# Performance work log

Hardware: AMD Instinct MI355X
Metric: run time of the kernel (lower is better)

## Reference

```python
import jax, jax.numpy as jnp
import numpy as np

N_NODES = 100000


def gcn_conv(x, W, b, src, dst, dinv):
    # PyG GCNConv with default add_self_loops=True, symmetric normalization.
    # x: [N, Fin], W: [Fin, Fout]. Self-loop contribution handled analytically
    # (norm for loop edge i->i is dinv[i]^2) instead of materializing loop edges.
    xw = x @ W                                   # [N, Fout]
    norm = dinv[src] * dinv[dst]                 # [E]
    msgs = xw[src] * norm[:, None]               # [E, Fout]
    agg = jax.ops.segment_sum(msgs, dst, num_segments=N_NODES)
    agg = agg + xw * (dinv * dinv)[:, None]      # self-loops
    return agg + b


def setup_inputs() -> dict:
    key = jax.random.key(0)
    ks = jax.random.split(key, 12)
    E = 3200000
    S = 1000000
    F_in = 512
    x = jax.random.normal(ks[0], (N_NODES, F_in), dtype=jnp.float32)
    edge_index = jax.random.randint(ks[1], (2, E), 0, N_NODES, dtype=jnp.int64)
    samples = jax.random.randint(ks[2], (S, 2), 0, N_NODES, dtype=jnp.int64)

    def glorot(k, fi, fo):
        lim = float(np.sqrt(6.0 / (fi + fo)))
        return jax.random.uniform(k, (fi, fo), jnp.float32, -lim, lim)

    W1 = glorot(ks[3], F_in, 8)
    b1 = jnp.zeros((8,), jnp.float32)
    W2 = glorot(ks[4], 8, 16)
    b2 = jnp.zeros((16,), jnp.float32)
    W3 = glorot(ks[5], 16, 32)
    b3 = jnp.zeros((32,), jnp.float32)
    Wfc = glorot(ks[6], 64, 1)
    bfc = jnp.zeros((1,), jnp.float32)
    return {"x": x, "edge_index": edge_index, "samples": samples,
            "W1": W1, "b1": b1, "W2": W2, "b2": b2, "W3": W3, "b3": b3,
            "Wfc": Wfc, "bfc": bfc}


def reference(x, edge_index, samples, W1, b1, W2, b2, W3, b3, Wfc, bfc):
    src, dst = edge_index[0], edge_index[1]
    # degree with self-loops (edge weight 1), deg >= 1 so rsqrt is safe
    deg = jax.ops.segment_sum(jnp.ones_like(src, dtype=x.dtype), dst,
                              num_segments=N_NODES) + 1.0
    dinv = jax.lax.rsqrt(deg)
    h = jax.nn.relu(gcn_conv(x, W1, b1, src, dst, dinv))
    h = jax.nn.relu(gcn_conv(h, W2, b2, src, dst, dinv))
    h = gcn_conv(h, W3, b3, src, dst, dinv)
    x_i = h[samples[:, 0]]                       # [S, 32]
    x_j = h[samples[:, 1]]                       # [S, 32]
    x_ij = jnp.concatenate([x_i, x_j], axis=1)   # [S, 64]
    return jax.nn.sigmoid(x_ij @ Wfc + bfc).squeeze(-1)
```

## Files before the change

kernel.cpp:

```cpp
#include <hip/hip_runtime.h>
#include <cstdint>

#define N_NODES 100000
#define NBKT 2048
#define KNODE 49
#define NBLK 256
#define TPB_P 512
#define CAP  2048


__global__ void k_hist(const int* __restrict__ dst, int* __restrict__ hist, int E) {
    __shared__ int h[NBKT];
    for (int i = threadIdx.x; i < NBKT; i += blockDim.x) h[i] = 0;
    __syncthreads();
    int chunk = (E + NBLK - 1) / NBLK;
    int lo = blockIdx.x * chunk, hi = min(lo + chunk, E);
    for (int i = lo + threadIdx.x; i < hi; i += blockDim.x)
        atomicAdd(&h[dst[i] / KNODE], 1);
    __syncthreads();
    int* hr = hist + (size_t)blockIdx.x * NBKT;
    for (int i = threadIdx.x; i < NBKT; i += blockDim.x) hr[i] = h[i];
}


__global__ void k_offs(const int* __restrict__ hist, int* __restrict__ offs,
                       int* __restrict__ btot) {
    int bkt = (blockIdx.x * blockDim.x + threadIdx.x) >> 6;
    if (bkt >= NBKT) return;
    int lane = threadIdx.x & 63;
    int vals[4], loc[4];
    int s = 0;
#pragma unroll
    for (int j = 0; j < 4; ++j) {
        int rr = lane * 4 + j;
        int r = ((rr & 31) << 3) | (rr >> 5);
        vals[j] = hist[(size_t)r * NBKT + bkt];
        loc[j] = s;
        s += vals[j];
    }
    int inc = s;
#pragma unroll
    for (int off = 1; off < 64; off <<= 1) {
        int u = __shfl_up(inc, off);
        if (lane >= off) inc += u;
    }
    int excl = inc - s;
#pragma unroll
    for (int j = 0; j < 4; ++j) {
        int rr = lane * 4 + j;
        int r = ((rr & 31) << 3) | (rr >> 5);
        offs[(size_t)r * NBKT + bkt] = excl + loc[j];
    }
    if (lane == 63) btot[bkt] = excl + s;
}


__global__ void k_bktscan(const int* __restrict__ btot, int* __restrict__ bbase) {
    __shared__ int s[256];
    int t = threadIdx.x;
    int loc[8];
    int sum = 0;
#pragma unroll
    for (int j = 0; j < 8; ++j) { loc[j] = btot[t * 8 + j]; sum += loc[j]; }
    s[t] = sum;
    __syncthreads();
    for (int off = 1; off < 256; off <<= 1) {
        int v = (t >= off) ? s[t - off] : 0;
        __syncthreads();
        s[t] += v;
        __syncthreads();
    }
    int base = s[t] - sum;
#pragma unroll
    for (int j = 0; j < 8; ++j) { bbase[t * 8 + j] = base; base += loc[j]; }
    if (t == 255) bbase[NBKT] = base;
}


__global__ void k_place(const int* __restrict__ src, const int* __restrict__ dst,
                        const int* __restrict__ offs, const int* __restrict__ bbase,
                        int* __restrict__ tmp, int E) {
    __shared__ int cur[NBKT];
    const int* orow = offs + (size_t)blockIdx.x * NBKT;
    for (int i = threadIdx.x; i < NBKT; i += blockDim.x) cur[i] = bbase[i] + orow[i];
    __syncthreads();
    int chunk = (E + NBLK - 1) / NBLK;
    int lo = blockIdx.x * chunk, hi = min(lo + chunk, E);
    for (int i = lo + threadIdx.x; i < hi; i += blockDim.x) {
        int d = dst[i], s = src[i];
        int b = d / KNODE;
        int p = atomicAdd(&cur[b], 1);
        tmp[p] = (s << 6) | (d - b * KNODE);
    }
}


__global__ void k_finalize(const int* __restrict__ tmp, const int* __restrict__ bbase,
                           int* __restrict__ row_start, float* __restrict__ dinv,
                           int* __restrict__ csr, int n) {
    __shared__ int sE[CAP];
    __shared__ int cnt[KNODE];
    __shared__ int pfx[KNODE];
    __shared__ int cur[KNODE];
    int b = blockIdx.x;
    int t = threadIdx.x;
    for (int i = t; i < KNODE; i += blockDim.x) cnt[i] = 0;
    __syncthreads();
    int n0 = bbase[b], n1 = bbase[b + 1];
    int m = n1 - n0;
    for (int i = t; i < m; i += blockDim.x) {
        int e = tmp[n0 + i];
        if (i < CAP) sE[i] = e;
        atomicAdd(&cnt[e & 63], 1);
    }
    __syncthreads();
    if (t == 0) {
        int run = n0;
        for (int j = 0; j < KNODE; ++j) { pfx[j] = run; run += cnt[j]; }
    }
    __syncthreads();
    if (t < KNODE) {
        int node = b * KNODE + t;
        if (node < n) {
            row_start[node] = pfx[t];
            dinv[node] = rsqrtf((float)cnt[t] + 1.0f);
        }
        cur[t] = pfx[t];
    }
    if (b == 0 && t == 0) row_start[n] = bbase[NBKT];
    __syncthreads();
    for (int i = t; i < m; i += blockDim.x) {
        int e = (i < CAP) ? sE[i] : tmp[n0 + i];
        int pos = atomicAdd(&cur[e & 63], 1);
        csr[pos] = e >> 6;
    }
}


__global__ void k_gemm1(const float* __restrict__ x, const float* __restrict__ W,
                        const float* __restrict__ dinv, float* __restrict__ xw, int n) {
    __shared__ float sWT[8 * 512];
    for (int i = threadIdx.x; i < 4096; i += blockDim.x) {
        int k = i >> 3, c = i & 7;
        sWT[c * 512 + k] = W[i];
    }
    __syncthreads();
    int wid = (blockIdx.x * blockDim.x + threadIdx.x) >> 6;
    int lane = threadIdx.x & 63;
    int r_sub = lane >> 3, j = lane & 7;
    int row = wid * 8 + r_sub;
    if (row >= n) return;
    const float* xr = x + (size_t)row * 512;
    float acc[8];
#pragma unroll
    for (int c = 0; c < 8; ++c) acc[c] = 0.f;
#pragma unroll 4
    for (int it = 0; it < 16; ++it) {
        int kb = it * 32 + j * 4;
        float4 v = *(const float4*)(xr + kb);
#pragma unroll
        for (int c = 0; c < 8; ++c) {
            const float* wt = &sWT[c * 512 + kb];
            acc[c] += v.x * wt[0] + v.y * wt[1] + v.z * wt[2] + v.w * wt[3];
        }
    }
#pragma unroll
    for (int off = 1; off < 8; off <<= 1)
#pragma unroll
        for (int c = 0; c < 8; ++c)
            acc[c] += __shfl_xor(acc[c], off);
    float outv = acc[0];
#pragma unroll
    for (int c = 1; c < 8; ++c) if (j == c) outv = acc[c];
    xw[(size_t)row * 8 + j] = outv * dinv[row];
}


__global__ void k_gather1(const float* __restrict__ xw, const int* __restrict__ csr,
                          const int* __restrict__ row_start, const float* __restrict__ dinv,
                          const float* __restrict__ b, float* __restrict__ out, int n) {
    int wid = (blockIdx.x * blockDim.x + threadIdx.x) >> 6;
    int lane = threadIdx.x & 63;
    if (wid >= n) return;
    int e = lane >> 3, c = lane & 7;
    int k0 = row_start[wid], k1 = row_start[wid + 1];
    float acc = 0.f;
    for (int k = k0 + e; k < k1; k += 8)
        acc += xw[(size_t)csr[k] * 8 + c];
    if (e == 0) acc += xw[(size_t)wid * 8 + c];
#pragma unroll
    for (int off = 8; off < 64; off <<= 1) acc += __shfl_xor(acc, off);
    if (lane < 8) {
        float di = dinv[wid];
        out[(size_t)wid * 8 + c] = fmaxf(acc * di + b[c], 0.f) * di;
    }
}


__global__ void k_gather2(const float* __restrict__ h1, const int* __restrict__ csr,
                          const int* __restrict__ row_start, const float* __restrict__ dinv,
                          const float* __restrict__ W2, const float* __restrict__ b2,
                          float* __restrict__ h2, int n) {
    __shared__ float sW[8 * 16];
    __shared__ float sB[16];
    if (threadIdx.x < 128) sW[threadIdx.x] = W2[threadIdx.x];
    if (threadIdx.x < 16) sB[threadIdx.x] = b2[threadIdx.x];
    __syncthreads();
    int wid = (blockIdx.x * blockDim.x + threadIdx.x) >> 6;
    int lane = threadIdx.x & 63;
    if (wid >= n) return;
    int e = lane >> 3, c = lane & 7;
    int k0 = row_start[wid], k1 = row_start[wid + 1];
    float acc = 0.f;
    for (int k = k0 + e; k < k1; k += 8)
        acc += h1[(size_t)csr[k] * 8 + c];
    if (e == 0) acc += h1[(size_t)wid * 8 + c];
#pragma unroll
    for (int off = 8; off < 64; off <<= 1) acc += __shfl_xor(acc, off);
    float di = dinv[wid];
    acc *= di;
    float s2[8];
#pragma unroll
    for (int k = 0; k < 8; ++k) s2[k] = __shfl(acc, k);
    if (lane < 16) {
        float a = sB[lane];
#pragma unroll
        for (int k = 0; k < 8; ++k) a += s2[k] * sW[k * 16 + lane];
        h2[(size_t)wid * 16 + lane] = fmaxf(a, 0.f) * di;
    }
}


__global__ void k_gather3(const float* __restrict__ h2, const int* __restrict__ csr,
                          const int* __restrict__ row_start, const float* __restrict__ dinv,
                          const float* __restrict__ v, const float* __restrict__ ch,
                          float* __restrict__ pi, float* __restrict__ pj, int n) {
    int wid = (blockIdx.x * blockDim.x + threadIdx.x) >> 6;
    int lane = threadIdx.x & 63;
    if (wid >= n) return;
    int e = lane >> 4, c = lane & 15;
    int k0 = row_start[wid], k1 = row_start[wid + 1];
    float acc = 0.f;
    for (int k = k0 + e; k < k1; k += 4)
        acc += h2[(size_t)csr[k] * 16 + c];
    if (e == 0) acc += h2[(size_t)wid * 16 + c];
#pragma unroll
    for (int off = 16; off < 64; off <<= 1) acc += __shfl_xor(acc, off);
    float t = acc * v[c];
    float u = acc * v[16 + c];
#pragma unroll
    for (int off = 1; off < 16; off <<= 1) {
        t += __shfl_xor(t, off);
        u += __shfl_xor(u, off);
    }
    if (lane == 0) {
        float di = dinv[wid];
        pi[wid] = t * di + ch[0];
        pj[wid] = u * di + ch[1];
    }
}


__global__ void k_prep_head(const float* __restrict__ W3, const float* __restrict__ b3,
                            const float* __restrict__ Wfc, float* __restrict__ v,
                            float* __restrict__ c) {
    int t = threadIdx.x;
    if (t < 32) {
        int j = t & 15;
        const float* wf = Wfc + (t < 16 ? 0 : 32);
        float a = 0.f;
        for (int k = 0; k < 32; ++k) a += W3[j * 32 + k] * wf[k];
        v[t] = a;
    } else if (t < 34) {
        const float* wf = Wfc + (t == 32 ? 0 : 32);
        float a = 0.f;
        for (int k = 0; k < 32; ++k) a += b3[k] * wf[k];
        c[t - 32] = a;
    }
}


__global__ void k_samples_fast(const int2* __restrict__ samples, const float* __restrict__ pi,
                               const float* __restrict__ pj, const float* __restrict__ bfc,
                               float* __restrict__ out, int S) {
    int i = blockIdx.x * blockDim.x + threadIdx.x;
    if (i >= S) return;
    int2 s = samples[i];
    float z = pi[s.x] + pj[s.y] + bfc[0];
    out[i] = 1.0f / (1.0f + __expf(-z));
}


extern "C" void kernel_launch(void* const* d_in, const int* in_sizes, int n_in,
                              void* d_out, int out_size, void* d_ws, size_t ws_size,
                              hipStream_t stream) {
    const float* x   = (const float*)d_in[0];
    const int*   ei  = (const int*)d_in[1];
    const int*   smp = (const int*)d_in[2];
    const float* W1  = (const float*)d_in[3];
    const float* b1  = (const float*)d_in[4];
    const float* W2  = (const float*)d_in[5];
    const float* b2  = (const float*)d_in[6];
    const float* W3  = (const float*)d_in[7];
    const float* b3  = (const float*)d_in[8];
    const float* Wfc = (const float*)d_in[9];
    const float* bfc = (const float*)d_in[10];
    float* out = (float*)d_out;

    const int E = in_sizes[1] / 2;
    const int S = in_sizes[2] / 2;
    const int N = N_NODES;
    const int* src = ei;
    const int* dst = ei + E;

    char* w = (char*)d_ws;
    size_t off = 0;
    auto alloc = [&](size_t bytes) {
        char* p = w + off;
        off += (bytes + 255) & ~(size_t)255;
        return p;
    };
    int*   row_start = (int*)alloc((N + 1) * 4);
    float* dinv      = (float*)alloc(N * 4);
    int*   csr       = (int*)alloc((size_t)E * 4);
    int*   btot      = (int*)alloc(NBKT * 4);
    int*   bbase     = (int*)alloc((NBKT + 1) * 4);

    size_t off_layers = off;
    float* xw1       = (float*)alloc((size_t)N * 8 * 4);
    float* h1        = (float*)alloc((size_t)N * 8 * 4);
    float* h2        = (float*)alloc((size_t)N * 16 * 4);
    float* vhead     = (float*)alloc(32 * 4);
    float* chead     = (float*)alloc(2 * 4);
    float* pi        = (float*)alloc(N * 4);
    float* pj        = (float*)alloc(N * 4);

    size_t tmp_off  = off_layers;
    size_t hist_off = tmp_off + (((size_t)E * 4 + 255) & ~(size_t)255);
    size_t offs_off = hist_off + (((size_t)NBLK * NBKT * 4 + 255) & ~(size_t)255);
    int* tmp  = (int*)(w + tmp_off);
    int* hist = (int*)(w + hist_off);
    int* offs = (int*)(w + offs_off);
    size_t scratch_end = offs_off + (size_t)NBLK * NBKT * 4;
    if (scratch_end > off) off = (scratch_end + 255) & ~(size_t)255;

    dim3 B(256);
    const int GN = (N * 64 + 255) / 256;

    k_hist<<<dim3(NBLK), dim3(TPB_P), 0, stream>>>(dst, hist, E);
    k_offs<<<dim3(NBKT * 64 / 256), B, 0, stream>>>(hist, offs, btot);
    k_bktscan<<<dim3(1), B, 0, stream>>>(btot, bbase);
    k_place<<<dim3(NBLK), dim3(TPB_P), 0, stream>>>(src, dst, offs, bbase, tmp, E);
    k_finalize<<<dim3(NBKT), B, 0, stream>>>(tmp, bbase, row_start, dinv, csr, N);

    k_gemm1<<<dim3(((N + 7) / 8 * 64 + 255) / 256), B, 0, stream>>>(x, W1, dinv, xw1, N);
    k_gather1<<<dim3(GN), B, 0, stream>>>(xw1, csr, row_start, dinv, b1, h1, N);

    k_gather2<<<dim3(GN), B, 0, stream>>>(h1, csr, row_start, dinv, W2, b2, h2, N);

    k_prep_head<<<dim3(1), dim3(64), 0, stream>>>(W3, b3, Wfc, vhead, chead);
    k_gather3<<<dim3(GN), B, 0, stream>>>(h2, csr, row_start, dinv, vhead, chead, pi, pj, N);

    k_samples_fast<<<dim3((S + 255) / 256), B, 0, stream>>>((const int2*)smp, pi, pj, bfc, out, S);
}
```

Before: 611.9 us.

## Fuse all stages into one persistent cooperative kernel with grid syncs

Replaces eleven separate kernel launches with a single cooperative persistent kernel of 512 blocks that moves between stages using grid-wide syncs. Stages use grid-stride loops and share one union of shared memory, and the head weights are now computed inside the kernel. The aim is to remove launch gaps and inter-kernel drain between the many small stages. The risk is lower occupancy with a fixed grid for the bandwidth-heavy gemm and gather stages, plus the cost of each grid.sync. Histogram partitioning also changes from 256 to 512 chunks.

```diff
diff --git a/kernel.cpp b/kernel.cpp
--- a/kernel.cpp
+++ b/kernel.cpp
@@ -1,293 +1,274 @@
 #include <hip/hip_runtime.h>
+#include <hip/hip_cooperative_groups.h>
 #include <cstdint>
+
+namespace cg = cooperative_groups;
 
 #define N_NODES 100000
 #define NBKT 2048
 #define KNODE 49
-#define NBLK 256
-#define TPB_P 512
-#define CAP  2048
-
-
-__global__ void k_hist(const int* __restrict__ dst, int* __restrict__ hist, int E) {
-    __shared__ int h[NBKT];
-    for (int i = threadIdx.x; i < NBKT; i += blockDim.x) h[i] = 0;
-    __syncthreads();
-    int chunk = (E + NBLK - 1) / NBLK;
-    int lo = blockIdx.x * chunk, hi = min(lo + chunk, E);
-    for (int i = lo + threadIdx.x; i < hi; i += blockDim.x)
-        atomicAdd(&h[dst[i] / KNODE], 1);
-    __syncthreads();
-    int* hr = hist + (size_t)blockIdx.x * NBKT;
-    for (int i = threadIdx.x; i < NBKT; i += blockDim.x) hr[i] = h[i];
-}
-
-
-__global__ void k_offs(const int* __restrict__ hist, int* __restrict__ offs,
-                       int* __restrict__ btot) {
-    int bkt = (blockIdx.x * blockDim.x + threadIdx.x) >> 6;
-    if (bkt >= NBKT) return;
-    int lane = threadIdx.x & 63;
-    int vals[4], loc[4];
-    int s = 0;
-#pragma unroll
-    for (int j = 0; j < 4; ++j) {
-        int rr = lane * 4 + j;
-        int r = ((rr & 31) << 3) | (rr >> 5);
-        vals[j] = hist[(size_t)r * NBKT + bkt];
-        loc[j] = s;
-        s += vals[j];
-    }
-    int inc = s;
-#pragma unroll
-    for (int off = 1; off < 64; off <<= 1) {
-        int u = __shfl_up(inc, off);
-        if (lane >= off) inc += u;
-    }
-    int excl = inc - s;
-#pragma unroll
-    for (int j = 0; j < 4; ++j) {
-        int rr = lane * 4 + j;
-        int r = ((rr & 31) << 3) | (rr >> 5);
-        offs[(size_t)r * NBKT + bkt] = excl + loc[j];
-    }
-    if (lane == 63) btot[bkt] = excl + s;
-}
-
-
-__global__ void k_bktscan(const int* __restrict__ btot, int* __restrict__ bbase) {
-    __shared__ int s[256];
-    int t = threadIdx.x;
-    int loc[8];
-    int sum = 0;
-#pragma unroll
-    for (int j = 0; j < 8; ++j) { loc[j] = btot[t * 8 + j]; sum += loc[j]; }
-    s[t] = sum;
-    __syncthreads();
-    for (int off = 1; off < 256; off <<= 1) {
-        int v = (t >= off) ? s[t - off] : 0;
-        __syncthreads();
-        s[t] += v;
-        __syncthreads();
-    }
-    int base = s[t] - sum;
-#pragma unroll
-    for (int j = 0; j < 8; ++j) { bbase[t * 8 + j] = base; base += loc[j]; }
-    if (t == 255) bbase[NBKT] = base;
-}
-
-
-__global__ void k_place(const int* __restrict__ src, const int* __restrict__ dst,
-                        const int* __restrict__ offs, const int* __restrict__ bbase,
-                        int* __restrict__ tmp, int E) {
-    __shared__ int cur[NBKT];
-    const int* orow = offs + (size_t)blockIdx.x * NBKT;
-    for (int i = threadIdx.x; i < NBKT; i += blockDim.x) cur[i] = bbase[i] + orow[i];
-    __syncthreads();
-    int chunk = (E + NBLK - 1) / NBLK;
-    int lo = blockIdx.x * chunk, hi = min(lo + chunk, E);
-    for (int i = lo + threadIdx.x; i < hi; i += blockDim.x) {
-        int d = dst[i], s = src[i];
-        int b = d / KNODE;
-        int p = atomicAdd(&cur[b], 1);
-        tmp[p] = (s << 6) | (d - b * KNODE);
-    }
-}
-
-
-__global__ void k_finalize(const int* __restrict__ tmp, const int* __restrict__ bbase,
-                           int* __restrict__ row_start, float* __restrict__ dinv,
-                           int* __restrict__ csr, int n) {
-    __shared__ int sE[CAP];
-    __shared__ int cnt[KNODE];
-    __shared__ int pfx[KNODE];
-    __shared__ int cur[KNODE];
-    int b = blockIdx.x;
-    int t = threadIdx.x;
-    for (int i = t; i < KNODE; i += blockDim.x) cnt[i] = 0;
-    __syncthreads();
-    int n0 = bbase[b], n1 = bbase[b + 1];
-    int m = n1 - n0;
-    for (int i = t; i < m; i += blockDim.x) {
-        int e = tmp[n0 + i];
-        if (i < CAP) sE[i] = e;
-        atomicAdd(&cnt[e & 63], 1);
-    }
-    __syncthreads();
-    if (t == 0) {
-        int run = n0;
-        for (int j = 0; j < KNODE; ++j) { pfx[j] = run; run += cnt[j]; }
-    }
-    __syncthreads();
-    if (t < KNODE) {
-        int node = b * KNODE + t;
-        if (node < n) {
-            row_start[node] = pfx[t];
-            dinv[node] = rsqrtf((float)cnt[t] + 1.0f);
-        }
-        cur[t] = pfx[t];
-    }
-    if (b == 0 && t == 0) row_start[n] = bbase[NBKT];
-    __syncthreads();
-    for (int i = t; i < m; i += blockDim.x) {
-        int e = (i < CAP) ? sE[i] : tmp[n0 + i];
-        int pos = atomicAdd(&cur[e & 63], 1);
-        csr[pos] = e >> 6;
-    }
-}
-
-
-__global__ void k_gemm1(const float* __restrict__ x, const float* __restrict__ W,
-                        const float* __restrict__ dinv, float* __restrict__ xw, int n) {
-    __shared__ float sWT[8 * 512];
-    for (int i = threadIdx.x; i < 4096; i += blockDim.x) {
-        int k = i >> 3, c = i & 7;
-        sWT[c * 512 + k] = W[i];
-    }
-    __syncthreads();
-    int wid = (blockIdx.x * blockDim.x + threadIdx.x) >> 6;
-    int lane = threadIdx.x & 63;
-    int r_sub = lane >> 3, j = lane & 7;
-    int row = wid * 8 + r_sub;
-    if (row >= n) return;
-    const float* xr = x + (size_t)row * 512;
-    float acc[8];
-#pragma unroll
-    for (int c = 0; c < 8; ++c) acc[c] = 0.f;
+#define GB 512
+#define TB 256
+#define NWAVE (GB * TB / 64)
+#define CAP 2048
+
+union SMem {
+    int ih[NBKT];
+    int sc[256];
+    struct { int sE[CAP]; int cnt[64]; int pfx[64]; int cur[64]; } fin;
+    float wt[8 * 512];
+    struct { float w[128]; float b[16]; } g2;
+    struct { float v[32]; float c2[2]; } g3;
+};
+
+struct Params {
+    const float* x; const int* src; const int* dst; const int2* smp;
+    const float* W1; const float* b1; const float* W2; const float* b2;
+    const float* W3; const float* b3; const float* Wfc; const float* bfc;
+    float* out;
+    int E; int S;
+    int* hist; int* offs; int* tmp; int* btot; int* bbase;
+    int* row_start; float* dinv; int* csr;
+    float* xw1; float* h1; float* h2; float* pi; float* pj;
+};
+
+__global__ __launch_bounds__(TB) void mega(Params p) {
+    cg::grid_group grid = cg::this_grid();
+    __shared__ SMem sm;
+    const int tid = threadIdx.x;
+    const int bid = blockIdx.x;
+    const int wid = (bid * TB + tid) >> 6;
+    const int lane = tid & 63;
+
+    for (int i = tid; i < NBKT; i += TB) sm.ih[i] = 0;
+    __syncthreads();
+    const int chunk = (p.E + GB - 1) / GB;
+    const int lo = bid * chunk, hi = min(lo + chunk, p.E);
+    for (int i = lo + tid; i < hi; i += TB)
+        atomicAdd(&sm.ih[p.dst[i] / KNODE], 1);
+    __syncthreads();
+    for (int i = tid; i < NBKT; i += TB) p.hist[(size_t)bid * NBKT + i] = sm.ih[i];
+    grid.sync();
+
+    {
+        int bkt = wid;
+        int vals[8], loc[8];
+        int s = 0;
+#pragma unroll
+        for (int j = 0; j < 8; ++j) {
+            int rr = lane * 8 + j;
+            int r = ((rr & 63) << 3) | (rr >> 6);
+            vals[j] = p.hist[(size_t)r * NBKT + bkt];
+            loc[j] = s; s += vals[j];
+        }
+        int inc = s;
+#pragma unroll
+        for (int o = 1; o < 64; o <<= 1) { int u = __shfl_up(inc, o); if (lane >= o) inc += u; }
+        int excl = inc - s;
+#pragma unroll
+        for (int j = 0; j < 8; ++j) {
+            int rr = lane * 8 + j;
+            int r = ((rr & 63) << 3) | (rr >> 6);
+            p.offs[(size_t)r * NBKT + bkt] = excl + loc[j];
+        }
+        if (lane == 63) p.btot[bkt] = excl + s;
+    }
+    grid.sync();
+
+    if (bid == 0) {
+        int loc[8], sum = 0;
+#pragma unroll
+        for (int j = 0; j < 8; ++j) { loc[j] = p.btot[tid * 8 + j]; sum += loc[j]; }
+        sm.sc[tid] = sum;
+        __syncthreads();
+        for (int o = 1; o < 256; o <<= 1) {
+            int v = (tid >= o) ? sm.sc[tid - o] : 0;
+            __syncthreads(); sm.sc[tid] += v; __syncthreads();
+        }
+        int base = sm.sc[tid] - sum;
+#pragma unroll
+        for (int j = 0; j < 8; ++j) { p.bbase[tid * 8 + j] = base; base += loc[j]; }
+        if (tid == 255) p.bbase[NBKT] = base;
+    }
+    grid.sync();
+
+    {
+        const int* orow = p.offs + (size_t)bid * NBKT;
+        for (int i = tid; i < NBKT; i += TB) sm.ih[i] = p.bbase[i] + orow[i];
+        __syncthreads();
+        for (int i = lo + tid; i < hi; i += TB) {
+            int d = p.dst[i], s = p.src[i];
+            int b = d / KNODE;
+            int pos = atomicAdd(&sm.ih[b], 1);
+            p.tmp[pos] = (s << 6) | (d - b * KNODE);
+        }
+    }
+    grid.sync();
+
+    for (int bi = 0; bi < NBKT / GB; ++bi) {
+        int b = bid * (NBKT / GB) + bi;
+        __syncthreads();
+        if (tid < 64) sm.fin.cnt[tid] = 0;
+        __syncthreads();
+        int n0 = p.bbase[b], n1 = p.bbase[b + 1];
+        int m = n1 - n0;
+        for (int i = tid; i < m; i += TB) {
+            int e = p.tmp[n0 + i];
+            if (i < CAP) sm.fin.sE[i] = e;
+            atomicAdd(&sm.fin.cnt[e & 63], 1);
+        }
+        __syncthreads();
+        if (tid == 0) {
+            int run = n0;
+            for (int j = 0; j < KNODE; ++j) { sm.fin.pfx[j] = run; run += sm.fin.cnt[j]; }
+        }
+        __syncthreads();
+        if (tid < KNODE) {
+            int node = b * KNODE + tid;
+            if (node < N_NODES) {
+                p.row_start[node] = sm.fin.pfx[tid];
+                p.dinv[node] = rsqrtf((float)sm.fin.cnt[tid] + 1.0f);
+            }
+            sm.fin.cur[tid] = sm.fin.pfx[tid];
+        }
+        if (b == 0 && tid == 0) p.row_start[N_NODES] = p.bbase[NBKT];
+        __syncthreads();
+        for (int i = tid; i < m; i += TB) {
+            int e = (i < CAP) ? sm.fin.sE[i] : p.tmp[n0 + i];
+            int pos = atomicAdd(&sm.fin.cur[e & 63], 1);
+            p.csr[pos] = e >> 6;
+        }
+    }
+    grid.sync();
+
+    __syncthreads();
+    for (int i = tid; i < 4096; i += TB) { int k = i >> 3, c = i & 7; sm.wt[c * 512 + k] = p.W1[i]; }
+    __syncthreads();
+    {
+        int r_sub = lane >> 3, j = lane & 7;
+        for (int rg = wid; rg < N_NODES / 8; rg += NWAVE) {
+            int row = rg * 8 + r_sub;
+            const float* xr = p.x + (size_t)row * 512;
+            float acc[8];
+#pragma unroll
+            for (int c = 0; c < 8; ++c) acc[c] = 0.f;
 #pragma unroll 4
-    for (int it = 0; it < 16; ++it) {
-        int kb = it * 32 + j * 4;
-        float4 v = *(const float4*)(xr + kb);
-#pragma unroll
-        for (int c = 0; c < 8; ++c) {
-            const float* wt = &sWT[c * 512 + kb];
-            acc[c] += v.x * wt[0] + v.y * wt[1] + v.z * wt[2] + v.w * wt[3];
-        }
-    }
-#pragma unroll
-    for (int off = 1; off < 8; off <<= 1)
-#pragma unroll
-        for (int c = 0; c < 8; ++c)
-            acc[c] += __shfl_xor(acc[c], off);
-    float outv = acc[0];
-#pragma unroll
-    for (int c = 1; c < 8; ++c) if (j == c) outv = acc[c];
-    xw[(size_t)row * 8 + j] = outv * dinv[row];
-}
-
-
-__global__ void k_gather1(const float* __restrict__ xw, const int* __restrict__ csr,
-                          const int* __restrict__ row_start, const float* __restrict__ dinv,
-                          const float* __restrict__ b, float* __restrict__ out, int n) {
-    int wid = (blockIdx.x * blockDim.x + threadIdx.x) >> 6;
-    int lane = threadIdx.x & 63;
-    if (wid >= n) return;
-    int e = lane >> 3, c = lane & 7;
-    int k0 = row_start[wid], k1 = row_start[wid + 1];
-    float acc = 0.f;
-    for (int k = k0 + e; k < k1; k += 8)
-        acc += xw[(size_t)csr[k] * 8 + c];
-    if (e == 0) acc += xw[(size_t)wid * 8 + c];
-#pragma unroll
-    for (int off = 8; off < 64; off <<= 1) acc += __shfl_xor(acc, off);
-    if (lane < 8) {
-        float di = dinv[wid];
-        out[(size_t)wid * 8 + c] = fmaxf(acc * di + b[c], 0.f) * di;
-    }
-}
-
-
-__global__ void k_gather2(const float* __restrict__ h1, const int* __restrict__ csr,
-                          const int* __restrict__ row_start, const float* __restrict__ dinv,
-                          const float* __restrict__ W2, const float* __restrict__ b2,
-                          float* __restrict__ h2, int n) {
-    __shared__ float sW[8 * 16];
-    __shared__ float sB[16];
-    if (threadIdx.x < 128) sW[threadIdx.x] = W2[threadIdx.x];
-    if (threadIdx.x < 16) sB[threadIdx.x] = b2[threadIdx.x];
-    __syncthreads();
-    int wid = (blockIdx.x * blockDim.x + threadIdx.x) >> 6;
-    int lane = threadIdx.x & 63;
-    if (wid >= n) return;
-    int e = lane >> 3, c = lane & 7;
-    int k0 = row_start[wid], k1 = row_start[wid + 1];
-    float acc = 0.f;
-    for (int k = k0 + e; k < k1; k += 8)
-        acc += h1[(size_t)csr[k] * 8 + c];
-    if (e == 0) acc += h1[(size_t)wid * 8 + c];
-#pragma unroll
-    for (int off = 8; off < 64; off <<= 1) acc += __shfl_xor(acc, off);
-    float di = dinv[wid];
-    acc *= di;
-    float s2[8];
-#pragma unroll
-    for (int k = 0; k < 8; ++k) s2[k] = __shfl(acc, k);
-    if (lane < 16) {
-        float a = sB[lane];
-#pragma unroll
-        for (int k = 0; k < 8; ++k) a += s2[k] * sW[k * 16 + lane];
-        h2[(size_t)wid * 16 + lane] = fmaxf(a, 0.f) * di;
-    }
-}
-
-
-__global__ void k_gather3(const float* __restrict__ h2, const int* __restrict__ csr,
-                          const int* __restrict__ row_start, const float* __restrict__ dinv,
-                          const float* __restrict__ v, const float* __restrict__ ch,
-                          float* __restrict__ pi, float* __restrict__ pj, int n) {
-    int wid = (blockIdx.x * blockDim.x + threadIdx.x) >> 6;
-    int lane = threadIdx.x & 63;
-    if (wid >= n) return;
-    int e = lane >> 4, c = lane & 15;
-    int k0 = row_start[wid], k1 = row_start[wid + 1];
-    float acc = 0.f;
-    for (int k = k0 + e; k < k1; k += 4)
-        acc += h2[(size_t)csr[k] * 16 + c];
-    if (e == 0) acc += h2[(size_t)wid * 16 + c];
-#pragma unroll
-    for (int off = 16; off < 64; off <<= 1) acc += __shfl_xor(acc, off);
-    float t = acc * v[c];
-    float u = acc * v[16 + c];
-#pragma unroll
-    for (int off = 1; off < 16; off <<= 1) {
-        t += __shfl_xor(t, off);
-        u += __shfl_xor(u, off);
-    }
-    if (lane == 0) {
-        float di = dinv[wid];
-        pi[wid] = t * di + ch[0];
-        pj[wid] = u * di + ch[1];
-    }
-}
-
-
-__global__ void k_prep_head(const float* __restrict__ W3, const float* __restrict__ b3,
-                            const float* __restrict__ Wfc, float* __restrict__ v,
-                            float* __restrict__ c) {
-    int t = threadIdx.x;
-    if (t < 32) {
-        int j = t & 15;
-        const float* wf = Wfc + (t < 16 ? 0 : 32);
+            for (int it = 0; it < 16; ++it) {
+                int kb = it * 32 + j * 4;
+                float4 v = *(const float4*)(xr + kb);
+#pragma unroll
+                for (int c = 0; c < 8; ++c) {
+                    const float* wt = &sm.wt[c * 512 + kb];
+                    acc[c] += v.x * wt[0] + v.y * wt[1] + v.z * wt[2] + v.w * wt[3];
+                }
+            }
+#pragma unroll
+            for (int o = 1; o < 8; o <<= 1)
+#pragma unroll
+                for (int c = 0; c < 8; ++c) acc[c] += __shfl_xor(acc[c], o);
+            float outv = acc[0];
+#pragma unroll
+            for (int c = 1; c < 8; ++c) if (j == c) outv = acc[c];
+            p.xw1[(size_t)row * 8 + j] = outv * p.dinv[row];
+        }
+    }
+    grid.sync();
+
+    {
+        int e8 = lane >> 3, c = lane & 7;
+        for (int node = wid; node < N_NODES; node += NWAVE) {
+            int k0 = p.row_start[node], k1 = p.row_start[node + 1];
+            float acc = 0.f;
+            for (int k = k0 + e8; k < k1; k += 8)
+                acc += p.xw1[(size_t)p.csr[k] * 8 + c];
+            if (e8 == 0) acc += p.xw1[(size_t)node * 8 + c];
+#pragma unroll
+            for (int o = 8; o < 64; o <<= 1) acc += __shfl_xor(acc, o);
+            if (lane < 8) {
+                float di = p.dinv[node];
+                p.h1[(size_t)node * 8 + c] = fmaxf(acc * di + p.b1[c], 0.f) * di;
+            }
+        }
+    }
+    grid.sync();
+
+    __syncthreads();
+    if (tid < 128) sm.g2.w[tid] = p.W2[tid];
+    if (tid < 16) sm.g2.b[tid] = p.b2[tid];
+    __syncthreads();
+    {
+        int e8 = lane >> 3, c = lane & 7;
+        for (int node = wid; node < N_NODES; node += NWAVE) {
+            int k0 = p.row_start[node], k1 = p.row_start[node + 1];
+            float acc = 0.f;
+            for (int k = k0 + e8; k < k1; k += 8)
+                acc += p.h1[(size_t)p.csr[k] * 8 + c];
+            if (e8 == 0) acc += p.h1[(size_t)node * 8 + c];
+#pragma unroll
+            for (int o = 8; o < 64; o <<= 1) acc += __shfl_xor(acc, o);
+            float di = p.dinv[node];
+            acc *= di;
+            float s2[8];
+#pragma unroll
+            for (int k = 0; k < 8; ++k) s2[k] = __shfl(acc, k);
+            if (lane < 16) {
+                float a = sm.g2.b[lane];
+#pragma unroll
+                for (int k = 0; k < 8; ++k) a += s2[k] * sm.g2.w[k * 16 + lane];
+                p.h2[(size_t)node * 16 + lane] = fmaxf(a, 0.f) * di;
+            }
+        }
+    }
+    grid.sync();
+
+    __syncthreads();
+    if (tid < 32) {
+        int j = tid & 15;
+        const float* wf = p.Wfc + (tid < 16 ? 0 : 32);
         float a = 0.f;
-        for (int k = 0; k < 32; ++k) a += W3[j * 32 + k] * wf[k];
-        v[t] = a;
-    } else if (t < 34) {
-        const float* wf = Wfc + (t == 32 ? 0 : 32);
+        for (int k = 0; k < 32; ++k) a += p.W3[j * 32 + k] * wf[k];
+        sm.g3.v[tid] = a;
+    } else if (tid < 34) {
+        const float* wf = p.Wfc + (tid == 32 ? 0 : 32);
         float a = 0.f;
-        for (int k = 0; k < 32; ++k) a += b3[k] * wf[k];
-        c[t - 32] = a;
-    }
-}
-
-
-__global__ void k_samples_fast(const int2* __restrict__ samples, const float* __restrict__ pi,
-                               const float* __restrict__ pj, const float* __restrict__ bfc,
-                               float* __restrict__ out, int S) {
-    int i = blockIdx.x * blockDim.x + threadIdx.x;
-    if (i >= S) return;
-    int2 s = samples[i];
-    float z = pi[s.x] + pj[s.y] + bfc[0];
-    out[i] = 1.0f / (1.0f + __expf(-z));
+        for (int k = 0; k < 32; ++k) a += p.b3[k] * wf[k];
+        sm.g3.c2[tid - 32] = a;
+    }
+    __syncthreads();
+    {
+        int e4 = lane >> 4, c = lane & 15;
+        for (int node = wid; node < N_NODES; node += NWAVE) {
+            int k0 = p.row_start[node], k1 = p.row_start[node + 1];
+            float acc = 0.f;
+            for (int k = k0 + e4; k < k1; k += 4)
+                acc += p.h2[(size_t)p.csr[k] * 16 + c];
+            if (e4 == 0) acc += p.h2[(size_t)node * 16 + c];
+#pragma unroll
+            for (int o = 16; o < 64; o <<= 1) acc += __shfl_xor(acc, o);
+            float t = acc * sm.g3.v[c];
+            float u = acc * sm.g3.v[16 + c];
+#pragma unroll
+            for (int o = 1; o < 16; o <<= 1) {
+                t += __shfl_xor(t, o);
+                u += __shfl_xor(u, o);
+            }
+            if (lane == 0) {
+                float di = p.dinv[node];
+                p.pi[node] = t * di + sm.g3.c2[0];
+                p.pj[node] = u * di + sm.g3.c2[1];
+            }
+        }
+    }
+    grid.sync();
+
+    {
+        float bfc0 = p.bfc[0];
+        for (int i = bid * TB + tid; i < p.S; i += GB * TB) {
+            int2 s = p.smp[i];
+            float z = p.pi[s.x] + p.pj[s.y] + bfc0;
+            p.out[i] = 1.0f / (1.0f + __expf(-z));
+        }
+    }
 }
 
 
@@ -297,21 +278,10 @@
     const float* x   = (const float*)d_in[0];
     const int*   ei  = (const int*)d_in[1];
     const int*   smp = (const int*)d_in[2];
-    const float* W1  = (const float*)d_in[3];
-    const float* b1  = (const float*)d_in[4];
-    const float* W2  = (const float*)d_in[5];
-    const float* b2  = (const float*)d_in[6];
-    const float* W3  = (const float*)d_in[7];
-    const float* b3  = (const float*)d_in[8];
-    const float* Wfc = (const float*)d_in[9];
-    const float* bfc = (const float*)d_in[10];
-    float* out = (float*)d_out;
 
     const int E = in_sizes[1] / 2;
     const int S = in_sizes[2] / 2;
     const int N = N_NODES;
-    const int* src = ei;
-    const int* dst = ei + E;
 
     char* w = (char*)d_ws;
     size_t off = 0;
@@ -330,36 +300,30 @@
     float* xw1       = (float*)alloc((size_t)N * 8 * 4);
     float* h1        = (float*)alloc((size_t)N * 8 * 4);
     float* h2        = (float*)alloc((size_t)N * 16 * 4);
-    float* vhead     = (float*)alloc(32 * 4);
-    float* chead     = (float*)alloc(2 * 4);
     float* pi        = (float*)alloc(N * 4);
     float* pj        = (float*)alloc(N * 4);
 
     size_t tmp_off  = off_layers;
     size_t hist_off = tmp_off + (((size_t)E * 4 + 255) & ~(size_t)255);
-    size_t offs_off = hist_off + (((size_t)NBLK * NBKT * 4 + 255) & ~(size_t)255);
+    size_t offs_off = hist_off + (((size_t)GB * NBKT * 4 + 255) & ~(size_t)255);
     int* tmp  = (int*)(w + tmp_off);
     int* hist = (int*)(w + hist_off);
     int* offs = (int*)(w + offs_off);
-    size_t scratch_end = offs_off + (size_t)NBLK * NBKT * 4;
+    size_t scratch_end = offs_off + (size_t)GB * NBKT * 4;
     if (scratch_end > off) off = (scratch_end + 255) & ~(size_t)255;
 
-    dim3 B(256);
-    const int GN = (N * 64 + 255) / 256;
-
-    k_hist<<<dim3(NBLK), dim3(TPB_P), 0, stream>>>(dst, hist, E);
-    k_offs<<<dim3(NBKT * 64 / 256), B, 0, stream>>>(hist, offs, btot);
-    k_bktscan<<<dim3(1), B, 0, stream>>>(btot, bbase);
-    k_place<<<dim3(NBLK), dim3(TPB_P), 0, stream>>>(src, dst, offs, bbase, tmp, E);
-    k_finalize<<<dim3(NBKT), B, 0, stream>>>(tmp, bbase, row_start, dinv, csr, N);
-
-    k_gemm1<<<dim3(((N + 7) / 8 * 64 + 255) / 256), B, 0, stream>>>(x, W1, dinv, xw1, N);
-    k_gather1<<<dim3(GN), B, 0, stream>>>(xw1, csr, row_start, dinv, b1, h1, N);
-
-    k_gather2<<<dim3(GN), B, 0, stream>>>(h1, csr, row_start, dinv, W2, b2, h2, N);
-
-    k_prep_head<<<dim3(1), dim3(64), 0, stream>>>(W3, b3, Wfc, vhead, chead);
-    k_gather3<<<dim3(GN), B, 0, stream>>>(h2, csr, row_start, dinv, vhead, chead, pi, pj, N);
-
-    k_samples_fast<<<dim3((S + 255) / 256), B, 0, stream>>>((const int2*)smp, pi, pj, bfc, out, S);
+    Params prm;
+    prm.x = x; prm.src = ei; prm.dst = ei + E; prm.smp = (const int2*)smp;
+    prm.W1 = (const float*)d_in[3];  prm.b1 = (const float*)d_in[4];
+    prm.W2 = (const float*)d_in[5];  prm.b2 = (const float*)d_in[6];
+    prm.W3 = (const float*)d_in[7];  prm.b3 = (const float*)d_in[8];
+    prm.Wfc = (const float*)d_in[9]; prm.bfc = (const float*)d_in[10];
+    prm.out = (float*)d_out;
+    prm.E = E; prm.S = S;
+    prm.hist = hist; prm.offs = offs; prm.tmp = tmp; prm.btot = btot; prm.bbase = bbase;
+    prm.row_start = row_start; prm.dinv = dinv; prm.csr = csr;
+    prm.xw1 = xw1; prm.h1 = h1; prm.h2 = h2; prm.pi = pi; prm.pj = pj;
+
+    void* args[] = { &prm };
+    hipLaunchCooperativeKernel((const void*)mega, dim3(GB), dim3(TB), args, 0, stream);
 }
```

Result: slower. 1.459 ms (+138.5%).
